# Optimization experiments

Measured on AMD Instinct MI355X. Metric: run time of the kernel, lower is better.

The kernel has to match this reference:

```python
import jax, jax.numpy as jnp
import numpy as np
from jax import lax

B, N, C = 2, 4096, 128
HEADS = 4
HD = C // HEADS
EXP = 2  # FFN_expand
EPS = 1e-5


def layernorm(x, w, b):
    mu = jnp.mean(x, axis=-1, keepdims=True)
    var = jnp.mean(jnp.square(x - mu), axis=-1, keepdims=True)
    return (x - mu) * lax.rsqrt(var + EPS) * w + b


def conv2d(x, w, b, pad, groups=1):
    # x: [B, Cin, H, W], w: [Cout, Cin//groups, kh, kw]
    y = lax.conv_general_dilated(
        x, w, window_strides=(1, 1), padding=[(pad, pad), (pad, pad)],
        dimension_numbers=('NCHW', 'OIHW', 'NCHW'), feature_group_count=groups)
    return y + b[None, :, None, None]


def setup_inputs() -> dict:
    key = jax.random.key(0)
    ks = jax.random.split(key, 16)
    C2 = C * EXP
    inp = {
        'x': jax.random.normal(ks[0], (B, N, C), jnp.float32),
        'H': 64,
        'W': 64,
        'ln1_w': jnp.ones((C,), jnp.float32),
        'ln1_b': jnp.zeros((C,), jnp.float32),
        'q_w': jax.random.normal(ks[1], (C, C), jnp.float32) * 0.02,
        'kv_w': jax.random.normal(ks[2], (2 * C, C), jnp.float32) * 0.02,
        'proj_w': jax.random.normal(ks[3], (C, C), jnp.float32) * 0.02,
        'proj_b': jnp.zeros((C,), jnp.float32),
        'ln2_w': jnp.ones((C,), jnp.float32),
        'ln2_b': jnp.zeros((C,), jnp.float32),
        'conv1_w': jax.random.normal(ks[4], (C2, C, 1, 1), jnp.float32) * np.sqrt(2.0 / C2),
        'conv1_b': jnp.zeros((C2,), jnp.float32),
        'conv33_w': jax.random.normal(ks[5], (C2, 1, 3, 3), jnp.float32) * np.sqrt(2.0 / 9),
        'conv33_b': jnp.zeros((C2,), jnp.float32),
        'conv55_w': jax.random.normal(ks[6], (C2, 1, 5, 5), jnp.float32) * np.sqrt(2.0 / 25),
        'conv55_b': jnp.zeros((C2,), jnp.float32),
        'conv4_w': jax.random.normal(ks[7], (C, C, 1, 1), jnp.float32) * np.sqrt(2.0 / C),
        'conv4_b': jnp.zeros((C,), jnp.float32),
    }
    return inp


def reference(x, H, W, ln1_w, ln1_b, q_w, kv_w, proj_w, proj_b,
              ln2_w, ln2_b, conv1_w, conv1_b, conv33_w, conv33_b,
              conv55_w, conv55_b, conv4_w, conv4_b):
    b, n, c = x.shape
    scale = HD ** -0.5

    # ---- Multi-head self-attention (sr_ratio=1) ----
    h = layernorm(x, ln1_w, ln1_b)
    q = jnp.einsum('bnc,oc->bno', h, q_w).reshape(b, n, HEADS, HD).transpose(0, 2, 1, 3)
    kv = jnp.einsum('bnc,oc->bno', h, kv_w).reshape(b, n, 2, HEADS, HD).transpose(2, 0, 3, 1, 4)
    k, v = kv[0], kv[1]
    attn = jnp.einsum('bhqd,bhkd->bhqk', q, k) * scale  # [B, heads, N, N]
    attn = jax.nn.softmax(attn, axis=-1)
    out = jnp.einsum('bhqk,bhkd->bhqd', attn, v).transpose(0, 2, 1, 3).reshape(b, n, c)
    out = jnp.einsum('bnc,oc->bno', out, proj_w) + proj_b
    x = x + out

    # ---- MFFN: conv1 + (dw3x3 + dw5x5) branches, SimpleGate, conv4 ----
    h = layernorm(x, ln2_w, ln2_b)
    hc = h.reshape(b, H, W, c).transpose(0, 3, 1, 2)  # NCHW
    x1 = conv2d(hc, conv1_w, conv1_b, pad=0)
    x33 = conv2d(x1, conv33_w, conv33_b, pad=1, groups=c * EXP)
    x55 = conv2d(x1, conv55_w, conv55_b, pad=2, groups=c * EXP)
    s = x1 + x33 + x55
    a, g = jnp.split(s, 2, axis=1)  # SimpleGate
    gated = a * g
    y = conv2d(gated, conv4_w, conv4_b, pad=0)
    y = y.transpose(0, 2, 3, 1).reshape(b, H * W, c)
    return x + y
```

## Files before the change

kernel.cpp:

```cpp
#include <hip/hip_runtime.h>
#include <hip/hip_bf16.h>
#include <math.h>

#define NB 2
#define NN 4096
#define NC 128
#define NH 4
#define HD 32
#define C2 256
#define HW 64
#define EPS 1e-5f

typedef unsigned short u16;
typedef short bf16x8 __attribute__((ext_vector_type(8)));
typedef unsigned short u16x8 __attribute__((ext_vector_type(8)));
typedef float f32x16 __attribute__((ext_vector_type(16)));

__device__ __forceinline__ u16 f2b(float x) {
    return __bfloat16_as_ushort(__float2bfloat16(x));
}
__device__ __forceinline__ float b2f(u16 v) {
    return __uint_as_float((unsigned)v << 16);
}
__device__ __forceinline__ unsigned pack_bf16(float a, float b) {
    return (unsigned)f2b(a) | ((unsigned)f2b(b) << 16);
}
__device__ __forceinline__ f32x16 fzero16() {
    f32x16 z;
    #pragma unroll
    for (int i = 0; i < 16; ++i) z[i] = 0.f;
    return z;
}
union U32x4 { unsigned u[4]; bf16x8 v; };

__device__ __forceinline__ void plswap(unsigned& a, unsigned& b) {
    asm("v_permlane32_swap_b32 %0, %1" : "+v"(a), "+v"(b));
}

__global__ void k_prep(const float* __restrict__ q_w, const float* __restrict__ kv_w,
                       const float* __restrict__ proj_w, const float* __restrict__ c1_w,
                       const float* __restrict__ c4_w, const float* __restrict__ c33_w,
                       const float* __restrict__ c55_w,
                       u16* wqkv, u16* wproj, u16* wc1, u16* wc4,
                       float* wt33, float* wt55) {
    const int tid = blockIdx.x * blockDim.x + threadIdx.x;
    const int nth = gridDim.x * blockDim.x;
    const float s = 0.17677669529663687f * 1.4426950408889634f;
    for (int i = tid; i < 128 * 128; i += nth) wqkv[i] = f2b(q_w[i] * s);
    for (int i = tid; i < 256 * 128; i += nth) wqkv[128 * 128 + i] = f2b(kv_w[i]);
    for (int i = tid; i < 128 * 128; i += nth) wproj[i] = f2b(proj_w[i]);
    for (int i = tid; i < 256 * 128; i += nth) wc1[i] = f2b(c1_w[i]);
    for (int i = tid; i < 128 * 128; i += nth) wc4[i] = f2b(c4_w[i]);
    for (int i = tid; i < 9 * 256; i += nth)  { int k = i >> 8, c = i & 255; wt33[i] = c33_w[c * 9 + k]; }
    for (int i = tid; i < 25 * 256; i += nth) { int k = i / 256, c = i % 256; wt55[i] = c55_w[c * 25 + k]; }
}

__global__ __launch_bounds__(256) void k_ln(
    const float* __restrict__ x, const float* __restrict__ w, const float* __restrict__ b,
    u16* __restrict__ h) {
    const int l = threadIdx.x & 63, wid = threadIdx.x >> 6;
    const int row = blockIdx.x * 4 + wid;
    const float2 xv = *(const float2*)(x + (size_t)row * NC + l * 2);
    float sum = xv.x + xv.y, ss = xv.x * xv.x + xv.y * xv.y;
    #pragma unroll
    for (int off = 1; off < 64; off <<= 1) {
        sum += __shfl_xor(sum, off);
        ss  += __shfl_xor(ss, off);
    }
    const float mean = sum * (1.0f / NC);
    const float var  = ss * (1.0f / NC) - mean * mean;
    const float rstd = rsqrtf(var + EPS);
    const float2 wv = *(const float2*)(w + l * 2);
    const float2 bv = *(const float2*)(b + l * 2);
    const float h0 = (xv.x - mean) * rstd * wv.x + bv.x;
    const float h1 = (xv.y - mean) * rstd * wv.y + bv.y;
    *(unsigned*)(h + (size_t)row * NC + l * 2) = pack_bf16(h0, h1);
}

__device__ __forceinline__ f32x16 gemm_tile_32x32(
    const u16* __restrict__ A, const u16* __restrict__ W, int m0, int n0, int q, int h5) {
    const u16* ap = A + (size_t)(m0 + q) * 128 + h5 * 8;
    const u16* wp = W + (size_t)(n0 + q) * 128 + h5 * 8;
    f32x16 acc = fzero16();
    #pragma unroll
    for (int kk = 0; kk < 8; ++kk) {
        bf16x8 af = *(const bf16x8*)(ap + kk * 16);
        bf16x8 wf = *(const bf16x8*)(wp + kk * 16);
        acc = __builtin_amdgcn_mfma_f32_32x32x16_bf16(af, wf, acc, 0, 0, 0);
    }
    return acc;
}
#define GEMM_PROLOG(NCOLS)                                    \
    const int l = threadIdx.x & 63, wid = threadIdx.x >> 6;   \
    const int q = l & 31, h5 = l >> 5;                        \
    const int m0 = blockIdx.x * 64 + (wid >> 1) * 32;         \
    const int n0 = blockIdx.y * 64 + (wid & 1) * 32;          \
    const int o = n0 + q;                                     \
    (void)o;

__global__ __launch_bounds__(256) void k_gemm_qkv(
    const u16* __restrict__ h1, const u16* __restrict__ wqkv,
    u16* __restrict__ qb, u16* __restrict__ kbuf, u16* __restrict__ vb) {
    GEMM_PROLOG(384)
    f32x16 acc = gemm_tile_32x32(h1, wqkv, m0, n0, q, h5);
    #pragma unroll
    for (int r = 0; r < 16; ++r) {
        const int mr = m0 + (r & 3) + 8 * (r >> 2) + 4 * h5;
        const int b_ = mr >> 12, n = mr & 4095;
        const u16 val = f2b(acc[r]);
        if (o < 128) {
            qb[((size_t)(b_ * 4 + (o >> 5)) * NN + n) * HD + (o & 31)] = val;
        } else if (o < 256) {
            const int o2 = o - 128;
            kbuf[((size_t)(b_ * 4 + (o2 >> 5)) * NN + n) * HD + (o2 & 31)] = val;
        } else {
            vb[(size_t)mr * 128 + (o - 256)] = val;
        }
    }
}

__global__ __launch_bounds__(256) void k_vt(const u16* __restrict__ vb, u16* __restrict__ vtb) {
    __shared__ u16 lds[32][64];
    const int t = threadIdx.x;
    const int bh = blockIdx.y, b_ = bh >> 2, hh = bh & 3;
    const int n0 = blockIdx.x * 64;
    {
        const int i = t >> 2, d0 = (t & 3) * 8;
        u16x8 v = *(const u16x8*)(vb + (size_t)(b_ * NN + n0 + i) * 128 + hh * 32 + d0);
        #pragma unroll
        for (int j = 0; j < 8; ++j) lds[d0 + j][i] = v[j];
    }
    __syncthreads();
    {
        const int d = t >> 3, j0 = (t & 7) * 8;
        u16x8 v;
        #pragma unroll
        for (int u = 0; u < 8; ++u) v[u] = lds[d][j0 + u];
        *(u16x8*)(vtb + ((size_t)bh * 32 + d) * NN + n0 + j0) = v;
    }
}

__global__ __launch_bounds__(256, 4) void k_attn(
    const u16* __restrict__ qb, const u16* __restrict__ kbuf, const u16* __restrict__ vtb,
    u16* __restrict__ ctxb) {
    __shared__ float sl[4][32];
    __shared__ float so[4][64][17];

    const int l = threadIdx.x & 63, w = threadIdx.x >> 6;
    const int q = l & 31, h5 = l >> 5;
    const int bh = blockIdx.x;
    const int qbase = blockIdx.y * 32;

    const u16* qp = qb + ((size_t)bh * NN + qbase + q) * HD + h5 * 8;
    const bf16x8 qf0 = *(const bf16x8*)qp;
    const bf16x8 qf1 = *(const bf16x8*)(qp + 16);

    bf16x8 ones;
    #pragma unroll
    for (int i = 0; i < 8; ++i) ones[i] = (short)0x3F80;

    const int kb0 = w * 1024;
    const u16* kp = kbuf + ((size_t)bh * NN + kb0 + q) * HD + h5 * 8;
    const u16* vp = vtb + ((size_t)bh * 32 + q) * NN + kb0 + h5 * 8;

    f32x16 O = fzero16();
    f32x16 L = fzero16();

    for (int t = 0; t < 32; ++t) {
        const bf16x8 kf0 = *(const bf16x8*)kp;
        const bf16x8 kf1 = *(const bf16x8*)(kp + 16);
        const bf16x8 vf0 = *(const bf16x8*)vp;
        const bf16x8 vf1 = *(const bf16x8*)(vp + 16);
        kp += 32 * HD;
        vp += 32;

        f32x16 s = fzero16();
        s = __builtin_amdgcn_mfma_f32_32x32x16_bf16(kf0, qf0, s, 0, 0, 0);
        s = __builtin_amdgcn_mfma_f32_32x32x16_bf16(kf1, qf1, s, 0, 0, 0);

        float p[16];
        #pragma unroll
        for (int r = 0; r < 16; ++r) p[r] = __builtin_amdgcn_exp2f(s[r]);

        unsigned pk[8];
        #pragma unroll
        for (int i = 0; i < 8; ++i) pk[i] = pack_bf16(p[2 * i], p[2 * i + 1]);
        U32x4 a0, a1;
        {
            unsigned x0 = pk[0], x2 = pk[2]; plswap(x0, x2);
            unsigned x1 = pk[1], x3 = pk[3]; plswap(x1, x3);
            a0.u[0] = x0; a0.u[1] = x1; a0.u[2] = x2; a0.u[3] = x3;
            unsigned y0 = pk[4], y2 = pk[6]; plswap(y0, y2);
            unsigned y1 = pk[5], y3 = pk[7]; plswap(y1, y3);
            a1.u[0] = y0; a1.u[1] = y1; a1.u[2] = y2; a1.u[3] = y3;
        }
        O = __builtin_amdgcn_mfma_f32_32x32x16_bf16(a0.v, vf0, O, 0, 0, 0);
        O = __builtin_amdgcn_mfma_f32_32x32x16_bf16(a1.v, vf1, O, 0, 0, 0);
        L = __builtin_amdgcn_mfma_f32_32x32x16_bf16(a0.v, ones, L, 0, 0, 0);
        L = __builtin_amdgcn_mfma_f32_32x32x16_bf16(a1.v, ones, L, 0, 0, 0);
    }

    if (q == 0) {
        #pragma unroll
        for (int r = 0; r < 16; ++r) sl[w][(r & 3) + 8 * (r >> 2) + 4 * h5] = L[r];
    }
    #pragma unroll
    for (int r = 0; r < 16; ++r) so[w][l][r] = O[r];
    __syncthreads();

    const int b_ = bh >> 2, h_ = bh & 3;
    #pragma unroll
    for (int i = 0; i < 4; ++i) {
        const int r = 4 * w + i;
        const int qr = (r & 3) + 8 * (r >> 2) + 4 * h5;
        const float os = so[0][l][r] + so[1][l][r] + so[2][l][r] + so[3][l][r];
        const float Lq = sl[0][qr] + sl[1][qr] + sl[2][qr] + sl[3][qr];
        ctxb[((size_t)(b_ * NN + qbase + qr)) * NC + h_ * 32 + q] = f2b(os / Lq);
    }
}

__global__ __launch_bounds__(256) void k_proj_ln(
    const u16* __restrict__ ctxb, const u16* __restrict__ wproj,
    const float* __restrict__ pbias, const float* __restrict__ x,
    const float* __restrict__ lnw, const float* __restrict__ lnb,
    float* __restrict__ x2, u16* __restrict__ h2) {
    __shared__ float sx[32][129];
    const int l = threadIdx.x & 63, wid = threadIdx.x >> 6;
    const int q = l & 31, h5 = l >> 5;
    const int m0 = blockIdx.x * 32;
    const int n0 = wid * 32;
    const int o = n0 + q;

    f32x16 acc = gemm_tile_32x32(ctxb, wproj, m0, n0, q, h5);
    const float bo = pbias[o];
    #pragma unroll
    for (int r = 0; r < 16; ++r) {
        const int rr = (r & 3) + 8 * (r >> 2) + 4 * h5;
        const int mr = m0 + rr;
        const float xv = acc[r] + bo + x[(size_t)mr * NC + o];
        x2[(size_t)mr * NC + o] = xv;
        sx[rr][o] = xv;
    }
    __syncthreads();

    const int t = threadIdx.x;
    const int row = t >> 3, cs = (t & 7) * 16;
    float vals[16];
    float sum = 0.f, ss = 0.f;
    #pragma unroll
    for (int i = 0; i < 16; ++i) {
        const float v = sx[row][cs + i];
        vals[i] = v; sum += v; ss += v * v;
    }
    #pragma unroll
    for (int off = 1; off < 8; off <<= 1) {
        sum += __shfl_xor(sum, off);
        ss  += __shfl_xor(ss, off);
    }
    const float mean = sum * (1.0f / NC);
    const float var  = ss * (1.0f / NC) - mean * mean;
    const float rstd = rsqrtf(var + EPS);
    const size_t base = (size_t)(m0 + row) * NC + cs;
    #pragma unroll
    for (int i = 0; i < 16; i += 2) {
        const float h0 = (vals[i]     - mean) * rstd * lnw[cs + i]     + lnb[cs + i];
        const float h1 = (vals[i + 1] - mean) * rstd * lnw[cs + i + 1] + lnb[cs + i + 1];
        *(unsigned*)(h2 + base + i) = pack_bf16(h0, h1);
    }
}

__global__ __launch_bounds__(256) void k_gemm_c1(
    const u16* __restrict__ h2, const u16* __restrict__ wc1,
    const float* __restrict__ bias, u16* __restrict__ x1) {
    GEMM_PROLOG(256)
    f32x16 acc = gemm_tile_32x32(h2, wc1, m0, n0, q, h5);
    const float bo = bias[o];
    #pragma unroll
    for (int r = 0; r < 16; ++r) {
        const int mr = m0 + (r & 3) + 8 * (r >> 2) + 4 * h5;
        x1[(size_t)mr * 256 + o] = f2b(acc[r] + bo);
    }
}

__global__ __launch_bounds__(128) void k_dwgate(
    const u16* __restrict__ x1, const float* __restrict__ wt33, const float* __restrict__ wt55,
    const float* __restrict__ b33, const float* __restrict__ b55, u16* __restrict__ gatedb) {
    const int pb = blockIdx.x, c = threadIdx.x;
    const int b_ = pb >> 12, p = pb & 4095;
    const int py = p >> 6, px = p & 63;
    const u16* base = x1 + (size_t)b_ * NN * C2;

    float a5 = 0.f, g5 = 0.f, a3 = 0.f, g3 = 0.f, ca = 0.f, cg = 0.f;
    #pragma unroll
    for (int dy = -2; dy <= 2; ++dy) {
        const int yy = py + dy;
        #pragma unroll
        for (int dx = -2; dx <= 2; ++dx) {
            const int xx = px + dx;
            const bool in = (yy >= 0) && (yy < HW) && (xx >= 0) && (xx < HW);
            const size_t off = (size_t)(yy * HW + xx) * C2;
            const float xa = in ? b2f(base[off + c]) : 0.f;
            const float xg = in ? b2f(base[off + 128 + c]) : 0.f;
            const int k5 = (dy + 2) * 5 + (dx + 2);
            a5 += xa * wt55[k5 * 256 + c];
            g5 += xg * wt55[k5 * 256 + 128 + c];
            if (dy >= -1 && dy <= 1 && dx >= -1 && dx <= 1) {
                const int k3 = (dy + 1) * 3 + (dx + 1);
                a3 += xa * wt33[k3 * 256 + c];
                g3 += xg * wt33[k3 * 256 + 128 + c];
            }
            if (dy == 0 && dx == 0) { ca = xa; cg = xg; }
        }
    }
    const float sa = ca + a3 + b33[c] + a5 + b55[c];
    const float sg = cg + g3 + b33[128 + c] + g5 + b55[128 + c];
    gatedb[(size_t)pb * 128 + c] = f2b(sa * sg);
}

__global__ __launch_bounds__(256) void k_gemm_c4(
    const u16* __restrict__ gatedb, const u16* __restrict__ wc4,
    const float* __restrict__ bias, const float* __restrict__ x2, float* __restrict__ out) {
    GEMM_PROLOG(128)
    f32x16 acc = gemm_tile_32x32(gatedb, wc4, m0, n0, q, h5);
    const float bo = bias[o];
    #pragma unroll
    for (int r = 0; r < 16; ++r) {
        const int mr = m0 + (r & 3) + 8 * (r >> 2) + 4 * h5;
        out[(size_t)mr * 128 + o] = acc[r] + bo + x2[(size_t)mr * 128 + o];
    }
}

extern "C" void kernel_launch(void* const* d_in, const int* in_sizes, int n_in,
                              void* d_out, int out_size, void* d_ws, size_t ws_size,
                              hipStream_t stream) {
    const float* x      = (const float*)d_in[0];
    const float* ln1_w  = (const float*)d_in[3];
    const float* ln1_b  = (const float*)d_in[4];
    const float* q_w    = (const float*)d_in[5];
    const float* kv_w   = (const float*)d_in[6];
    const float* proj_w = (const float*)d_in[7];
    const float* proj_b = (const float*)d_in[8];
    const float* ln2_w  = (const float*)d_in[9];
    const float* ln2_b  = (const float*)d_in[10];
    const float* c1_w   = (const float*)d_in[11];
    const float* c1_b   = (const float*)d_in[12];
    const float* c33_w  = (const float*)d_in[13];
    const float* c33_b  = (const float*)d_in[14];
    const float* c55_w  = (const float*)d_in[15];
    const float* c55_b  = (const float*)d_in[16];
    const float* c4_w   = (const float*)d_in[17];
    const float* c4_b   = (const float*)d_in[18];

    char* p = (char*)d_ws;
    u16*   wqkv  = (u16*)p;   p += 384 * 128 * 2;
    u16*   wproj = (u16*)p;   p += 128 * 128 * 2;
    u16*   wc1   = (u16*)p;   p += 256 * 128 * 2;
    u16*   wc4   = (u16*)p;   p += 128 * 128 * 2;
    float* wt33  = (float*)p; p += 9 * 256 * 4;
    float* wt55  = (float*)p; p += 25 * 256 * 4;
    u16*   h1    = (u16*)p;   p += (size_t)8192 * 128 * 2;
    u16*   qb    = (u16*)p;   p += (size_t)8 * 4096 * 32 * 2;
    u16*   kb    = (u16*)p;   p += (size_t)8 * 4096 * 32 * 2;
    u16*   vb    = (u16*)p;   p += (size_t)8192 * 128 * 2;
    u16*   vtb   = (u16*)p;   p += (size_t)8 * 32 * 4096 * 2;
    u16*   ctxb  = (u16*)p;   p += (size_t)8192 * 128 * 2;
    float* x2    = (float*)p; p += (size_t)8192 * 128 * 4;
    u16*   h2    = (u16*)p;   p += (size_t)8192 * 128 * 2;
    u16*   x1    = (u16*)p;   p += (size_t)8192 * 256 * 2;
    u16*   gatedb= (u16*)p;   p += (size_t)8192 * 128 * 2;
    float* out   = (float*)d_out;

    k_prep<<<64, 256, 0, stream>>>(q_w, kv_w, proj_w, c1_w, c4_w, c33_w, c55_w,
                                   wqkv, wproj, wc1, wc4, wt33, wt55);
    k_ln<<<2048, 256, 0, stream>>>(x, ln1_w, ln1_b, h1);
    k_gemm_qkv<<<dim3(128, 6), 256, 0, stream>>>(h1, wqkv, qb, kb, vb);
    k_vt<<<dim3(64, 8), 256, 0, stream>>>(vb, vtb);
    k_attn<<<dim3(NB * NH, NN / 32), 256, 0, stream>>>(qb, kb, vtb, ctxb);
    k_proj_ln<<<256, 256, 0, stream>>>(ctxb, wproj, proj_b, x, ln2_w, ln2_b, x2, h2);
    k_gemm_c1<<<dim3(128, 4), 256, 0, stream>>>(h2, wc1, c1_b, x1);
    k_dwgate<<<NB * NN, 128, 0, stream>>>(x1, wt33, wt55, c33_b, c55_b, gatedb);
    k_gemm_c4<<<dim3(128, 2), 256, 0, stream>>>(gatedb, wc4, c4_b, x2, out);
}
```

Baseline: 227.5 us.

## Fold depthwise convs into one 5x5 kernel and fuse V transpose into QKV GEMM

Combines the 3x3, 5x5 and identity branches into a single effective 5x5 depthwise weight with a summed bias, prepared in the setup kernel. The gate kernel is rewritten to process 4 channels per thread with vector loads across 8 pixels per block. The QKV GEMM epilogue now writes V directly in transposed layout, which removes the separate transpose kernel and its intermediate buffer. Storing the effective weights in bf16 adds rounding error on the merged taps.

```diff
diff --git a/kernel.cpp b/kernel.cpp
--- a/kernel.cpp
+++ b/kernel.cpp
@@ -40,9 +40,10 @@
 __global__ void k_prep(const float* __restrict__ q_w, const float* __restrict__ kv_w,
                        const float* __restrict__ proj_w, const float* __restrict__ c1_w,
                        const float* __restrict__ c4_w, const float* __restrict__ c33_w,
-                       const float* __restrict__ c55_w,
+                       const float* __restrict__ c55_w, const float* __restrict__ c33_b,
+                       const float* __restrict__ c55_b,
                        u16* wqkv, u16* wproj, u16* wc1, u16* wc4,
-                       float* wt33, float* wt55) {
+                       u16* weff, float* beff) {
     const int tid = blockIdx.x * blockDim.x + threadIdx.x;
     const int nth = gridDim.x * blockDim.x;
     const float s = 0.17677669529663687f * 1.4426950408889634f;
@@ -51,8 +52,16 @@
     for (int i = tid; i < 128 * 128; i += nth) wproj[i] = f2b(proj_w[i]);
     for (int i = tid; i < 256 * 128; i += nth) wc1[i] = f2b(c1_w[i]);
     for (int i = tid; i < 128 * 128; i += nth) wc4[i] = f2b(c4_w[i]);
-    for (int i = tid; i < 9 * 256; i += nth)  { int k = i >> 8, c = i & 255; wt33[i] = c33_w[c * 9 + k]; }
-    for (int i = tid; i < 25 * 256; i += nth) { int k = i / 256, c = i % 256; wt55[i] = c55_w[c * 25 + k]; }
+    for (int i = tid; i < 25 * 256; i += nth) {
+        const int k = i / 256, c = i % 256;
+        const int dy = k / 5 - 2, dx = k % 5 - 2;
+        float w = c55_w[c * 25 + k];
+        if (dy >= -1 && dy <= 1 && dx >= -1 && dx <= 1)
+            w += c33_w[c * 9 + (dy + 1) * 3 + (dx + 1)];
+        if (k == 12) w += 1.0f;
+        weff[k * 256 + c] = f2b(w);
+    }
+    for (int i = tid; i < 256; i += nth) beff[i] = c33_b[i] + c55_b[i];
 }
 
 __global__ __launch_bounds__(256) void k_ln(
@@ -100,43 +109,34 @@
 
 __global__ __launch_bounds__(256) void k_gemm_qkv(
     const u16* __restrict__ h1, const u16* __restrict__ wqkv,
-    u16* __restrict__ qb, u16* __restrict__ kbuf, u16* __restrict__ vb) {
+    u16* __restrict__ qb, u16* __restrict__ kbuf, u16* __restrict__ vtb) {
     GEMM_PROLOG(384)
     f32x16 acc = gemm_tile_32x32(h1, wqkv, m0, n0, q, h5);
-    #pragma unroll
-    for (int r = 0; r < 16; ++r) {
-        const int mr = m0 + (r & 3) + 8 * (r >> 2) + 4 * h5;
-        const int b_ = mr >> 12, n = mr & 4095;
-        const u16 val = f2b(acc[r]);
-        if (o < 128) {
-            qb[((size_t)(b_ * 4 + (o >> 5)) * NN + n) * HD + (o & 31)] = val;
-        } else if (o < 256) {
-            const int o2 = o - 128;
-            kbuf[((size_t)(b_ * 4 + (o2 >> 5)) * NN + n) * HD + (o2 & 31)] = val;
-        } else {
-            vb[(size_t)mr * 128 + (o - 256)] = val;
+    if (o < 256) {
+        #pragma unroll
+        for (int r = 0; r < 16; ++r) {
+            const int mr = m0 + (r & 3) + 8 * (r >> 2) + 4 * h5;
+            const int b_ = mr >> 12, n = mr & 4095;
+            const u16 val = f2b(acc[r]);
+            if (o < 128) {
+                qb[((size_t)(b_ * 4 + (o >> 5)) * NN + n) * HD + (o & 31)] = val;
+            } else {
+                const int o2 = o - 128;
+                kbuf[((size_t)(b_ * 4 + (o2 >> 5)) * NN + n) * HD + (o2 & 31)] = val;
+            }
         }
-    }
-}
-
-__global__ __launch_bounds__(256) void k_vt(const u16* __restrict__ vb, u16* __restrict__ vtb) {
-    __shared__ u16 lds[32][64];
-    const int t = threadIdx.x;
-    const int bh = blockIdx.y, b_ = bh >> 2, hh = bh & 3;
-    const int n0 = blockIdx.x * 64;
-    {
-        const int i = t >> 2, d0 = (t & 3) * 8;
-        u16x8 v = *(const u16x8*)(vb + (size_t)(b_ * NN + n0 + i) * 128 + hh * 32 + d0);
-        #pragma unroll
-        for (int j = 0; j < 8; ++j) lds[d0 + j][i] = v[j];
-    }
-    __syncthreads();
-    {
-        const int d = t >> 3, j0 = (t & 7) * 8;
-        u16x8 v;
-        #pragma unroll
-        for (int u = 0; u < 8; ++u) v[u] = lds[d][j0 + u];
-        *(u16x8*)(vtb + ((size_t)bh * 32 + d) * NN + n0 + j0) = v;
+    } else {
+        const int vo = o - 256;
+        const int hh = vo >> 5, d = vo & 31;
+        u16* vrow = vtb + ((size_t)((m0 >> 12) * 4 + hh) * 32 + d) * NN;
+        const int nb = (m0 & 4095) + 4 * h5;
+        #pragma unroll
+        for (int g = 0; g < 4; ++g) {
+            ushort4 pv;
+            pv.x = f2b(acc[4 * g + 0]); pv.y = f2b(acc[4 * g + 1]);
+            pv.z = f2b(acc[4 * g + 2]); pv.w = f2b(acc[4 * g + 3]);
+            *(ushort4*)(vrow + nb + 8 * g) = pv;
+        }
     }
 }
 
@@ -282,39 +282,46 @@
     }
 }
 
-__global__ __launch_bounds__(128) void k_dwgate(
-    const u16* __restrict__ x1, const float* __restrict__ wt33, const float* __restrict__ wt55,
-    const float* __restrict__ b33, const float* __restrict__ b55, u16* __restrict__ gatedb) {
-    const int pb = blockIdx.x, c = threadIdx.x;
+__global__ __launch_bounds__(256) void k_dwgate(
+    const u16* __restrict__ x1, const u16* __restrict__ weff, const float* __restrict__ beff,
+    u16* __restrict__ gatedb) {
+    const int t = threadIdx.x;
+    const int cg = (t & 31) * 4;
+    const int pb = blockIdx.x * 8 + (t >> 5);
     const int b_ = pb >> 12, p = pb & 4095;
     const int py = p >> 6, px = p & 63;
-    const u16* base = x1 + (size_t)b_ * NN * C2;
-
-    float a5 = 0.f, g5 = 0.f, a3 = 0.f, g3 = 0.f, ca = 0.f, cg = 0.f;
+    const u16* base = x1 + ((size_t)b_ * 4096 + p) * C2;
+
+    float a0 = 0.f, a1 = 0.f, a2 = 0.f, a3 = 0.f;
+    float g0 = 0.f, g1 = 0.f, g2 = 0.f, g3 = 0.f;
     #pragma unroll
     for (int dy = -2; dy <= 2; ++dy) {
         const int yy = py + dy;
+        const bool yin = (yy >= 0) && (yy < HW);
         #pragma unroll
         for (int dx = -2; dx <= 2; ++dx) {
             const int xx = px + dx;
-            const bool in = (yy >= 0) && (yy < HW) && (xx >= 0) && (xx < HW);
-            const size_t off = (size_t)(yy * HW + xx) * C2;
-            const float xa = in ? b2f(base[off + c]) : 0.f;
-            const float xg = in ? b2f(base[off + 128 + c]) : 0.f;
+            const bool in = yin && (xx >= 0) && (xx < HW);
             const int k5 = (dy + 2) * 5 + (dx + 2);
-            a5 += xa * wt55[k5 * 256 + c];
-            g5 += xg * wt55[k5 * 256 + 128 + c];
-            if (dy >= -1 && dy <= 1 && dx >= -1 && dx <= 1) {
-                const int k3 = (dy + 1) * 3 + (dx + 1);
-                a3 += xa * wt33[k3 * 256 + c];
-                g3 += xg * wt33[k3 * 256 + 128 + c];
-            }
-            if (dy == 0 && dx == 0) { ca = xa; cg = xg; }
+            const u16* xp = base + (dy * HW + dx) * C2;
+            ushort4 xa = in ? *(const ushort4*)(xp + cg) : ushort4{0, 0, 0, 0};
+            ushort4 xg = in ? *(const ushort4*)(xp + 128 + cg) : ushort4{0, 0, 0, 0};
+            const ushort4 wa = *(const ushort4*)(weff + k5 * 256 + cg);
+            const ushort4 wg = *(const ushort4*)(weff + k5 * 256 + 128 + cg);
+            a0 += b2f(xa.x) * b2f(wa.x); a1 += b2f(xa.y) * b2f(wa.y);
+            a2 += b2f(xa.z) * b2f(wa.z); a3 += b2f(xa.w) * b2f(wa.w);
+            g0 += b2f(xg.x) * b2f(wg.x); g1 += b2f(xg.y) * b2f(wg.y);
+            g2 += b2f(xg.z) * b2f(wg.z); g3 += b2f(xg.w) * b2f(wg.w);
         }
     }
-    const float sa = ca + a3 + b33[c] + a5 + b55[c];
-    const float sg = cg + g3 + b33[128 + c] + g5 + b55[128 + c];
-    gatedb[(size_t)pb * 128 + c] = f2b(sa * sg);
+    const float4 ba = *(const float4*)(beff + cg);
+    const float4 bg = *(const float4*)(beff + 128 + cg);
+    ushort4 o4;
+    o4.x = f2b((a0 + ba.x) * (g0 + bg.x));
+    o4.y = f2b((a1 + ba.y) * (g1 + bg.y));
+    o4.z = f2b((a2 + ba.z) * (g2 + bg.z));
+    o4.w = f2b((a3 + ba.w) * (g3 + bg.w));
+    *(ushort4*)(gatedb + (size_t)pb * 128 + cg) = o4;
 }
 
 __global__ __launch_bounds__(256) void k_gemm_c4(
@@ -356,12 +363,12 @@
     u16*   wproj = (u16*)p;   p += 128 * 128 * 2;
     u16*   wc1   = (u16*)p;   p += 256 * 128 * 2;
     u16*   wc4   = (u16*)p;   p += 128 * 128 * 2;
-    float* wt33  = (float*)p; p += 9 * 256 * 4;
-    float* wt55  = (float*)p; p += 25 * 256 * 4;
+    u16*   weff  = (u16*)p;   p += 25 * 256 * 2;
+    float* beff  = (float*)p; p += 256 * 4;
+    p = (char*)(((size_t)p + 255) & ~(size_t)255);
     u16*   h1    = (u16*)p;   p += (size_t)8192 * 128 * 2;
     u16*   qb    = (u16*)p;   p += (size_t)8 * 4096 * 32 * 2;
     u16*   kb    = (u16*)p;   p += (size_t)8 * 4096 * 32 * 2;
-    u16*   vb    = (u16*)p;   p += (size_t)8192 * 128 * 2;
     u16*   vtb   = (u16*)p;   p += (size_t)8 * 32 * 4096 * 2;
     u16*   ctxb  = (u16*)p;   p += (size_t)8192 * 128 * 2;
     float* x2    = (float*)p; p += (size_t)8192 * 128 * 4;
@@ -371,13 +378,12 @@
     float* out   = (float*)d_out;
 
     k_prep<<<64, 256, 0, stream>>>(q_w, kv_w, proj_w, c1_w, c4_w, c33_w, c55_w,
-                                   wqkv, wproj, wc1, wc4, wt33, wt55);
+                                   c33_b, c55_b, wqkv, wproj, wc1, wc4, weff, beff);
     k_ln<<<2048, 256, 0, stream>>>(x, ln1_w, ln1_b, h1);
-    k_gemm_qkv<<<dim3(128, 6), 256, 0, stream>>>(h1, wqkv, qb, kb, vb);
-    k_vt<<<dim3(64, 8), 256, 0, stream>>>(vb, vtb);
+    k_gemm_qkv<<<dim3(128, 6), 256, 0, stream>>>(h1, wqkv, qb, kb, vtb);
     k_attn<<<dim3(NB * NH, NN / 32), 256, 0, stream>>>(qb, kb, vtb, ctxb);
     k_proj_ln<<<256, 256, 0, stream>>>(ctxb, wproj, proj_b, x, ln2_w, ln2_b, x2, h2);
     k_gemm_c1<<<dim3(128, 4), 256, 0, stream>>>(h2, wc1, c1_b, x1);
-    k_dwgate<<<NB * NN, 128, 0, stream>>>(x1, wt33, wt55, c33_b, c55_b, gatedb);
+    k_dwgate<<<1024, 256, 0, stream>>>(x1, weff, beff, gatedb);
     k_gemm_c4<<<dim3(128, 2), 256, 0, stream>>>(gatedb, wc4, c4_b, x2, out);
 }
```

Result: faster. 221.8 us (-2.5%).
